# Optimization experiments

Hardware: AMD Instinct MI355X
Metric: run time of the kernel (lower is better)

The kernel has to match this reference:

```python
import jax, jax.numpy as jnp
import numpy as np

B, DIM, H, W = 8, 128, 64, 64
C, DI, N, R, K = DIM // 4, 2 * (DIM // 4), 16, 2, 4  # chunk dim, d_inner, d_state, dt_rank, n_dirs
L = H * W
EPS = 1e-5


def dwconv(x, w, b, dil):
    # x: [B,C,H,W]; w: [C,1,kh,kw] depthwise; torch padding='same' with dilation
    y = jax.lax.conv_general_dilated(
        x, w, window_strides=(1, 1), padding='SAME', rhs_dilation=(dil, dil),
        dimension_numbers=('NCHW', 'OIHW', 'NCHW'), feature_group_count=x.shape[1])
    return y + b[None, :, None, None]


def layernorm(x, w, b):
    mu = jnp.mean(x, -1, keepdims=True)
    var = jnp.var(x, -1, keepdims=True)
    return (x - mu) * jax.lax.rsqrt(var + EPS) * w + b


def axial_dw(x, mh_w, mh_b, mw_w, mw_b, c_w, c_b, dil):
    skip = x
    x = dwconv(x, mw_w, mw_b, dil)   # (1,7) kernel
    x = dwconv(x, mh_w, mh_b, dil)   # (7,1) kernel
    x = dwconv(x, c_w, c_b, dil)     # 3x3 kernel
    return x + skip


def ss2d(x, in_proj_w, conv_w, conv_b, x_proj_w, dt_proj_w, dt_proj_b,
         A_log, D, out_norm_w, out_norm_b, out_proj_w):
    # x: [B,H,W,C] channels-last (VMamba SS2D)
    b, h, w, _ = x.shape
    xz = jnp.einsum('bhwc,ec->bhwe', x, in_proj_w)          # [B,H,W,2*DI]
    xc, z = jnp.split(xz, 2, axis=-1)
    xc = xc.transpose(0, 3, 1, 2)                           # [B,DI,H,W]
    xc = jax.nn.silu(dwconv(xc, conv_w, conv_b, 1))
    l = h * w
    x_hw = xc.reshape(b, DI, l)
    x_wh = xc.transpose(0, 1, 3, 2).reshape(b, DI, l)
    xs = jnp.stack([x_hw, x_wh], 1)                         # [B,2,DI,L]
    xs = jnp.concatenate([xs, jnp.flip(xs, -1)], 1)         # [B,4,DI,L]
    x_dbl = jnp.einsum('bkdl,kcd->bkcl', xs, x_proj_w)      # c = R+2N
    dts, Bs, Cs = x_dbl[:, :, :R], x_dbl[:, :, R:R + N], x_dbl[:, :, R + N:]
    dts = jnp.einsum('bkrl,kdr->bkdl', dts, dt_proj_w)
    delta = jax.nn.softplus(dts + dt_proj_b[None, :, :, None])  # [B,4,DI,L]
    A = -jnp.exp(A_log)                                     # [4,DI,N]

    def step(hst, inp):
        u_t, dt_t, B_t, C_t = inp  # [B,4,DI],[B,4,DI],[B,4,N],[B,4,N]
        dA = jnp.exp(dt_t[..., None] * A)                   # [B,4,DI,N]
        hst = hst * dA + (dt_t * u_t)[..., None] * B_t[:, :, None, :]
        y = jnp.einsum('bkdn,bkn->bkd', hst, C_t)
        return hst, y

    u_l = jnp.moveaxis(xs, -1, 0)
    dt_l = jnp.moveaxis(delta, -1, 0)
    B_l = jnp.moveaxis(Bs, -1, 0)
    C_l = jnp.moveaxis(Cs, -1, 0)
    h0 = jnp.zeros((b, K, DI, N), xc.dtype)
    _, ys = jax.lax.scan(step, h0, (u_l, dt_l, B_l, C_l))   # [L,B,4,DI]
    out_y = jnp.moveaxis(ys, 0, -1) + D[None, :, :, None] * xs  # [B,4,DI,L]

    inv_y = jnp.flip(out_y[:, 2:4], -1)
    wh_y = out_y[:, 1].reshape(b, DI, w, h).transpose(0, 1, 3, 2).reshape(b, DI, l)
    invwh_y = inv_y[:, 1].reshape(b, DI, w, h).transpose(0, 1, 3, 2).reshape(b, DI, l)
    y = out_y[:, 0] + inv_y[:, 0] + wh_y + invwh_y          # [B,DI,L]
    y = y.transpose(0, 2, 1).reshape(b, h, w, DI)
    y = layernorm(y, out_norm_w, out_norm_b)
    y = y * jax.nn.silu(z)
    return jnp.einsum('bhwd,cd->bhwc', y, out_proj_w)


def setup_inputs() -> dict:
    key = jax.random.key(0)
    ks = iter(jax.random.split(key, 64))
    nrm = lambda s, sc=0.05: jax.random.normal(next(ks), s, jnp.float32) * sc
    inp = {'x': jax.random.normal(next(ks), (B, DIM, H, W), jnp.float32)}
    for i in (1, 2, 3):
        inp[f'dw{i}_mh_w'] = nrm((C, 1, 7, 1), 0.1); inp[f'dw{i}_mh_b'] = nrm((C,), 0.02)
        inp[f'dw{i}_mw_w'] = nrm((C, 1, 1, 7), 0.1); inp[f'dw{i}_mw_b'] = nrm((C,), 0.02)
        inp[f'dw{i}_c_w'] = nrm((C, 1, 3, 3), 0.1); inp[f'dw{i}_c_b'] = nrm((C,), 0.02)
    inp['ln_w'] = jnp.ones((C,)); inp['ln_b'] = jnp.zeros((C,))
    inp['in_proj_w'] = nrm((2 * DI, C))
    inp['conv_w'] = nrm((DI, 1, 3, 3), 0.1); inp['conv_b'] = nrm((DI,), 0.02)
    inp['x_proj_w'] = nrm((K, R + 2 * N, DI))
    inp['dt_proj_w'] = nrm((K, DI, R), 0.1)
    inp['dt_proj_b'] = nrm((K, DI), 0.02)
    inp['A_log'] = jax.random.uniform(next(ks), (K, DI, N), jnp.float32, 0.0, 2.0)
    inp['D'] = jnp.ones((K, DI), jnp.float32)
    inp['out_norm_w'] = jnp.ones((DI,)); inp['out_norm_b'] = jnp.zeros((DI,))
    inp['out_proj_w'] = nrm((C, DI))
    inp['bn_g'] = jnp.ones((DIM,)); inp['bn_b'] = jnp.zeros((DIM,))
    inp['bn_m'] = jnp.zeros((DIM,)); inp['bn_v'] = jnp.ones((DIM,))
    return inp


def reference(x, dw1_mh_w, dw1_mh_b, dw1_mw_w, dw1_mw_b, dw1_c_w, dw1_c_b,
              dw2_mh_w, dw2_mh_b, dw2_mw_w, dw2_mw_b, dw2_c_w, dw2_c_b,
              dw3_mh_w, dw3_mh_b, dw3_mw_w, dw3_mw_b, dw3_c_w, dw3_c_b,
              ln_w, ln_b, in_proj_w, conv_w, conv_b, x_proj_w, dt_proj_w, dt_proj_b,
              A_log, D, out_norm_w, out_norm_b, out_proj_w, bn_g, bn_b, bn_m, bn_v):
    def vss(xc):  # shared VSSBlock: [B,C,H,W] -> [B,C,H,W]
        t = xc.transpose(0, 2, 3, 1)
        t = t + ss2d(layernorm(t, ln_w, ln_b), in_proj_w, conv_w, conv_b, x_proj_w,
                     dt_proj_w, dt_proj_b, A_log, D, out_norm_w, out_norm_b, out_proj_w)
        return t.transpose(0, 3, 1, 2)

    x1, x2, x3, x4 = jnp.split(x, 4, axis=1)
    x1 = vss(axial_dw(x1, dw1_mh_w, dw1_mh_b, dw1_mw_w, dw1_mw_b, dw1_c_w, dw1_c_b, 1))
    x2 = vss(axial_dw(x2, dw2_mh_w, dw2_mh_b, dw2_mw_w, dw2_mw_b, dw2_c_w, dw2_c_b, 2))
    x3 = vss(axial_dw(x3, dw3_mh_w, dw3_mh_b, dw3_mw_w, dw3_mw_b, dw3_c_w, dw3_c_b, 3))
    xc = jnp.concatenate([x1, x2, x3, x4], axis=1)
    # BatchNorm2d in inference mode (running stats)
    y = (xc - bn_m[None, :, None, None]) * jax.lax.rsqrt(bn_v + EPS)[None, :, None, None]
    y = y * bn_g[None, :, None, None] + bn_b[None, :, None, None]
    return jax.nn.relu(y)
```

## Files before the change

### kernel.cpp

```cpp
#include <hip/hip_runtime.h>
#include <math.h>

#define LB __launch_bounds__(256)
#define LB512 __launch_bounds__(512)

#define LOG2E 1.44269504088896340736f
static __device__ __forceinline__ float silu_f(float x){ return x / (1.f + __expf(-x)); }
static __device__ __forceinline__ float softplus_f(float x){
    return (x > 20.f) ? x : __logf(1.f + __expf(x));
}

struct AxialArgs { const float* w[18]; };

__global__ LB void axial_kernel(const float* __restrict__ x, AxialArgs args,
                                float* __restrict__ acc)
{
    __shared__ float s0[4096];
    __shared__ float s1[4096];
    const int chunk = blockIdx.x >> 8;
    const int bc = blockIdx.x & 255;
    const int b = bc >> 5, c = bc & 31;
    const int dil = chunk + 1;
    const float* mh_w = args.w[chunk*6+0];
    const float* mh_b = args.w[chunk*6+1];
    const float* mw_w = args.w[chunk*6+2];
    const float* mw_b = args.w[chunk*6+3];
    const float* cw   = args.w[chunk*6+4];
    const float* cb   = args.w[chunk*6+5];
    const int tid = threadIdx.x;
    const float* xin = x + ((size_t)(b*128 + chunk*32 + c)) * 4096;
    float orig[16];
    #pragma unroll
    for (int kk=0;kk<16;++kk){ float v=xin[tid+kk*256]; orig[kk]=v; s0[tid+kk*256]=v; }
    __syncthreads();

    float w7[7];
    #pragma unroll
    for (int t=0;t<7;++t) w7[t]=mw_w[c*7+t];
    float bias = mw_b[c];
    float v[16];
    #pragma unroll
    for (int kk=0;kk<16;++kk){
        int p=tid+kk*256, i=p>>6, j=p&63;
        float s=bias;
        #pragma unroll
        for (int t=0;t<7;++t){ int jj=j+(t-3)*dil; if (jj>=0&&jj<64) s+=s0[i*64+jj]*w7[t]; }
        v[kk]=s;
    }
    #pragma unroll
    for (int kk=0;kk<16;++kk) s1[tid+kk*256]=v[kk];
    __syncthreads();

    #pragma unroll
    for (int t=0;t<7;++t) w7[t]=mh_w[c*7+t];
    bias = mh_b[c];
    #pragma unroll
    for (int kk=0;kk<16;++kk){
        int p=tid+kk*256, i=p>>6, j=p&63;
        float s=bias;
        #pragma unroll
        for (int t=0;t<7;++t){ int ii=i+(t-3)*dil; if (ii>=0&&ii<64) s+=s1[ii*64+j]*w7[t]; }
        v[kk]=s;
    }
    __syncthreads();
    #pragma unroll
    for (int kk=0;kk<16;++kk) s0[tid+kk*256]=v[kk];
    __syncthreads();

    float w9[9];
    #pragma unroll
    for (int t=0;t<9;++t) w9[t]=cw[c*9+t];
    bias = cb[c];
    float* aout = acc + (size_t)chunk*1048576 + ((size_t)(b*32+c))*4096;
    #pragma unroll
    for (int kk=0;kk<16;++kk){
        int p=tid+kk*256, i=p>>6, j=p&63;
        float s=bias;
        #pragma unroll
        for (int a=0;a<3;++a){
            int ii=i+(a-1)*dil; if (ii<0||ii>=64) continue;
            #pragma unroll
            for (int bb2=0;bb2<3;++bb2){
                int jj=j+(bb2-1)*dil; if (jj<0||jj>=64) continue;
                s += s0[ii*64+jj]*w9[a*3+bb2];
            }
        }
        aout[p] = s + orig[kk];
    }
}

__global__ LB512 void lnproj_kernel(const float* __restrict__ acc,
    const float* __restrict__ ln_w, const float* __restrict__ ln_b,
    const float* __restrict__ in_proj_w,
    float* __restrict__ xc, float* __restrict__ z)
{
    __shared__ float s_a[32*65];
    const int b = blockIdx.x >> 6, lt = blockIdx.x & 63;
    const int l0 = lt*64;
    const int tid = threadIdx.x;
    const float* ab = acc + (size_t)b*32*4096 + l0;
    for (int i=tid;i<2048;i+=512){ int c=i>>6, j=i&63; s_a[c*65+j]=ab[(size_t)c*4096 + j]; }
    __syncthreads();
    const int l = tid & 63;
    const int g = __builtin_amdgcn_readfirstlane(tid >> 6);
    float v[32];
    float mu=0.f;
    #pragma unroll
    for (int c=0;c<32;++c){ v[c]=s_a[c*65+l]; mu+=v[c]; }
    mu *= (1.f/32.f);
    float var=0.f;
    #pragma unroll
    for (int c=0;c<32;++c){ float d2=v[c]-mu; var+=d2*d2; }
    var *= (1.f/32.f);
    float rs = rsqrtf(var+1e-5f);
    #pragma unroll
    for (int c=0;c<32;++c) v[c] = (v[c]-mu)*rs*ln_w[c] + ln_b[c];
    float* xcp = xc + (size_t)b*64*4096 + l0 + l;
    float* zp  = z  + (size_t)b*64*4096 + l0 + l;
    for (int e=g*16; e<g*16+16; ++e){
        const float* wr = in_proj_w + e*32;
        float s=0.f;
        #pragma unroll
        for (int c=0;c<32;++c) s += wr[c]*v[c];
        if (e<64) xcp[(size_t)e*4096]=s; else zp[(size_t)(e-64)*4096]=s;
    }
}

__global__ LB void conv3_kernel(const float* __restrict__ xc,
    const float* __restrict__ conv_w, const float* __restrict__ conv_b,
    float* __restrict__ xconv, float* __restrict__ xconvT)
{
    __shared__ float s0[4096];
    __shared__ float s1[64*65];
    const int bd = blockIdx.x;
    const int d = bd & 63;
    const int tid = threadIdx.x;
    const float* in = xc + (size_t)bd*4096;
    #pragma unroll
    for (int kk=0;kk<16;++kk) s0[tid+kk*256]=in[tid+kk*256];
    __syncthreads();
    float w9[9];
    #pragma unroll
    for (int t=0;t<9;++t) w9[t]=conv_w[d*9+t];
    float bias = conv_b[d];
    float* outp = xconv + (size_t)bd*4096;
    #pragma unroll
    for (int kk=0;kk<16;++kk){
        int p=tid+kk*256, i=p>>6, j=p&63;
        float s=bias;
        #pragma unroll
        for (int a=0;a<3;++a){
            int ii=i+a-1; if (ii<0||ii>=64) continue;
            #pragma unroll
            for (int bb2=0;bb2<3;++bb2){
                int jj=j+bb2-1; if (jj<0||jj>=64) continue;
                s += s0[ii*64+jj]*w9[a*3+bb2];
            }
        }
        s = silu_f(s);
        outp[p]=s;
        s1[i*65+j]=s;
    }
    __syncthreads();
    float* outT = xconvT + (size_t)bd*4096;
    #pragma unroll
    for (int kk=0;kk<16;++kk){ int p=tid+kk*256; outT[p] = s1[(p&63)*65 + (p>>6)]; }
}

__global__ LB void projscan1_kernel(const float* __restrict__ xconv, const float* __restrict__ xconvT,
    const float* __restrict__ x_proj_w, const float* __restrict__ dt_proj_w,
    const float* __restrict__ dt_proj_b, const float* __restrict__ A_log,
    float* __restrict__ Bsb, float* __restrict__ Csb, float* __restrict__ dts_g,
    float* __restrict__ Ssum, float* __restrict__ hloc)
{
    __shared__ float s_x[64*65];
    __shared__ float s_dlt[64*65];
    __shared__ __align__(16) float s_B[1024];
    __shared__ float s_dts[128];
    __shared__ float s_Spart[4][64];
    float* s_C = s_dlt;
    const int blk = blockIdx.x;
    const int g = blk & 63, bk = blk >> 6;
    const int k = bk & 3, b = bk >> 2;
    const int tid = threadIdx.x;
    const int t0 = g*64;
    const float* src = (k & 1) ? xconvT : xconv;
    const float* sb = src + (size_t)b*64*4096;
    for (int i=tid;i<4096;i+=256){
        int d=i>>6, j=i&63;
        int col = (k&2) ? (4095-(t0+j)) : (t0+j);
        s_x[j*65+d] = sb[(size_t)d*4096 + col];
    }
    __syncthreads();

    {
        const int t = tid & 63;
        const int q = __builtin_amdgcn_readfirstlane(tid >> 6);
        const float* wp = x_proj_w + k*2176;
        float acc9[9];
        #pragma unroll
        for (int r=0;r<9;++r) acc9[r]=0.f;
        const int r0 = q*9;
        const int nr = (q==3)?7:9;
        for (int ch=0; ch<4; ++ch){
            float xv[16];
            #pragma unroll
            for (int i=0;i<16;++i) xv[i] = s_x[t*65 + ch*16 + i];
            #pragma unroll
            for (int r=0;r<9;++r){
                if (r < nr){
                    const float* wr = wp + (r0+r)*64 + ch*16;
                    float s=0.f;
                    #pragma unroll
                    for (int i=0;i<16;++i) s += wr[i]*xv[i];
                    acc9[r] += s;
                }
            }
        }
        #pragma unroll
        for (int r=0;r<9;++r){
            if (r<nr){
                int row = r0 + r;
                if (row < 2)       s_dts[t*2 + row]      = acc9[r];
                else if (row < 18) s_B[t*16 + (row-2)]   = acc9[r];
                else               s_C[t*16 + (row-18)]  = acc9[r];
            }
        }
    }
    __syncthreads();

    {
        const size_t tb = (size_t)blk*1024;
        for (int i=tid;i<1024;i+=256){ Bsb[tb+i]=s_B[i]; Csb[tb+i]=s_C[i]; }
        if (tid<128) dts_g[(size_t)blk*128 + tid] = s_dts[tid];
    }
    __syncthreads();

    {
        const int d_ = tid & 63, part = tid >> 6;
        const float w0 = dt_proj_w[k*128 + d_*2], w1 = dt_proj_w[k*128 + d_*2 + 1];
        const float bb = dt_proj_b[k*64 + d_];
        float Sp = 0.f;
        #pragma unroll
        for (int i=0;i<16;++i){
            const int t = part*16 + i;
            float dlt = softplus_f(s_dts[t*2]*w0 + s_dts[t*2+1]*w1 + bb);
            s_dlt[t*65 + d_] = dlt;
            s_x[t*65 + d_] *= dlt;
            Sp += dlt;
        }
        s_Spart[part][d_] = Sp;
    }
    __syncthreads();
    if (tid < 64){
        Ssum[(size_t)blk*64 + tid] = s_Spart[0][tid]+s_Spart[1][tid]
                                   + s_Spart[2][tid]+s_Spart[3][tid];
    }

    const int d = tid >> 2, nb = (tid & 3)*4;
    float4 Av = *(const float4*)(A_log + ((size_t)(k*64+d)*16 + nb));
    const float A0 = -__expf(Av.x)*LOG2E, A1 = -__expf(Av.y)*LOG2E,
                A2 = -__expf(Av.z)*LOG2E, A3 = -__expf(Av.w)*LOG2E;
    float h0=0,h1=0,h2=0,h3=0;
    #pragma unroll 4
    for (int t=0;t<64;++t){
        float dlt = s_dlt[t*65+d];
        float du  = s_x[t*65+d];
        float4 Bv = *(const float4*)&s_B[t*16+nb];
        h0 = h0*exp2f(dlt*A0) + du*Bv.x;
        h1 = h1*exp2f(dlt*A1) + du*Bv.y;
        h2 = h2*exp2f(dlt*A2) + du*Bv.z;
        h3 = h3*exp2f(dlt*A3) + du*Bv.w;
    }
    ((float4*)hloc)[(size_t)blk*256 + tid] = make_float4(h0,h1,h2,h3);
}

__global__ LB void scan2_kernel(const float* __restrict__ Ssum,
    const float* __restrict__ hloc, const float* __restrict__ A_log,
    float* __restrict__ hin)
{
    const int j = blockIdx.x*256 + threadIdx.x;
    const int bk = j >> 10, dn = j & 1023;
    const int k = bk & 3, d = dn >> 4, n = dn & 15;
    const float A = -__expf(A_log[(size_t)(k*64+d)*16 + n]) * LOG2E;
    float h = 0.f;
    for (int g=0; g<64; ++g){
        const size_t o = ((size_t)bk*64 + g)*1024 + dn;
        hin[o] = h;
        float S = Ssum[((size_t)bk*64 + g)*64 + d];
        h = exp2f(A*S)*h + hloc[o];
    }
}

__global__ LB void scan3_kernel(const float* __restrict__ xconv, const float* __restrict__ xconvT,
    const float* __restrict__ Bsb, const float* __restrict__ Csb,
    const float* __restrict__ dts_g,
    const float* __restrict__ dt_proj_w, const float* __restrict__ dt_proj_b,
    const float* __restrict__ A_log, const float* __restrict__ Dp,
    const float* __restrict__ hin, float* __restrict__ outy)
{
    __shared__ __align__(16) float s_B[4][1024];
    __shared__ __align__(16) float s_C[4][1024];
    __shared__ float s_dts[4][128];
    __shared__ float s_y[4][64*17];
    const int w = threadIdx.x >> 6;
    const int lane = threadIdx.x & 63;
    const int tile = blockIdx.x*4 + w;
    const int g = tile & 63, bk = tile >> 6;
    const int k = bk & 3, b = bk >> 2;

    {
        const float4* B4 = (const float4*)(Bsb + (size_t)tile*1024);
        const float4* C4 = (const float4*)(Csb + (size_t)tile*1024);
        float4* sB4 = (float4*)s_B[w];
        float4* sC4 = (float4*)s_C[w];
        #pragma unroll
        for (int qq=0;qq<4;++qq){ sB4[lane+64*qq]=B4[lane+64*qq]; sC4[lane+64*qq]=C4[lane+64*qq]; }
        s_dts[w][lane]      = dts_g[(size_t)tile*128 + lane];
        s_dts[w][lane+64]   = dts_g[(size_t)tile*128 + lane + 64];
    }
    const int d = lane;
    float A[16];
    {
        const float* Ab = A_log + (size_t)(k*64+d)*16;
        #pragma unroll
        for (int n=0;n<16;++n) A[n] = -__expf(Ab[n])*LOG2E;
    }
    float h[16];
    {
        const float4* hb = (const float4*)(hin + (size_t)tile*1024 + d*16);
        #pragma unroll
        for (int qq=0;qq<4;++qq){
            float4 v=hb[qq];
            h[qq*4+0]=v.x; h[qq*4+1]=v.y; h[qq*4+2]=v.z; h[qq*4+3]=v.w;
        }
    }
    const float w0 = dt_proj_w[k*128 + d*2], w1 = dt_proj_w[k*128 + d*2 + 1];
    const float bb = dt_proj_b[k*64 + d];
    const float Dv = Dp[k*64 + d];
    const float* up = ((k&1)?xconvT:xconv) + (size_t)(b*64+d)*4096;
    const float4* sB4 = (const float4*)s_B[w];
    const float4* sC4 = (const float4*)s_C[w];
    float* syw = s_y[w];

    for (int t4=0; t4<16; ++t4){
        float u4[4];
        if (k & 2){
            float4 r = *(const float4*)(up + (4092 - g*64 - t4*4));
            u4[0]=r.w; u4[1]=r.z; u4[2]=r.y; u4[3]=r.x;
        } else {
            float4 r = *(const float4*)(up + g*64 + t4*4);
            u4[0]=r.x; u4[1]=r.y; u4[2]=r.z; u4[3]=r.w;
        }
        #pragma unroll
        for (int j=0;j<4;++j){
            const int t = t4*4 + j;
            float dt0 = s_dts[w][t*2], dt1 = s_dts[w][t*2+1];
            float dlt = softplus_f(dt0*w0 + dt1*w1 + bb);
            float du  = dlt * u4[j];
            float y = 0.f;
            #pragma unroll
            for (int qq=0;qq<4;++qq){
                float4 Bv = sB4[t*4+qq];
                float4 Cv = sC4[t*4+qq];
                h[qq*4+0] = h[qq*4+0]*exp2f(dlt*A[qq*4+0]) + du*Bv.x;
                h[qq*4+1] = h[qq*4+1]*exp2f(dlt*A[qq*4+1]) + du*Bv.y;
                h[qq*4+2] = h[qq*4+2]*exp2f(dlt*A[qq*4+2]) + du*Bv.z;
                h[qq*4+3] = h[qq*4+3]*exp2f(dlt*A[qq*4+3]) + du*Bv.w;
                y += h[qq*4+0]*Cv.x + h[qq*4+1]*Cv.y + h[qq*4+2]*Cv.z + h[qq*4+3]*Cv.w;
            }
            syw[d*17 + (t & 15)] = y + Dv*u4[j];
        }
        if ((t4 & 3) == 3){
            const int tb = t4 >> 2;
            #pragma unroll
            for (int qq=0;qq<16;++qq){
                int i = qq*64 + lane;
                int dd = i >> 4, jj = i & 15;
                outy[((size_t)(bk*64+dd))*4096 + g*64 + tb*16 + jj] = syw[dd*17 + jj];
            }
        }
    }
}

__global__ LB void outyT_kernel(const float* __restrict__ outy, float* __restrict__ outyT)
{
    __shared__ float s[64*65];
    const int p = blockIdx.x;
    const int kk = p >> 9, bd = p & 511;
    const int b = bd >> 6, d = bd & 63;
    const float* ip = outy + ((size_t)(b*4 + (kk?3:1))*64 + d)*4096;
    const int tid = threadIdx.x;
    #pragma unroll
    for (int k2=0;k2<16;++k2){ int pp=tid+k2*256; s[(pp>>6)*65+(pp&63)] = ip[pp]; }
    __syncthreads();
    float* op = outyT + ((size_t)(kk*8+b)*64 + d)*4096;
    #pragma unroll
    for (int k2=0;k2<16;++k2){ int pp=tid+k2*256; op[pp] = s[(pp&63)*65 + (pp>>6)]; }
}

__global__ LB512 void combine_kernel(const float* __restrict__ outy,
    const float* __restrict__ outyT,
    const float* __restrict__ z, const float* __restrict__ acc,
    const float* __restrict__ onw, const float* __restrict__ onb,
    const float* __restrict__ opw,
    const float* __restrict__ bn_g, const float* __restrict__ bn_b,
    const float* __restrict__ bn_m, const float* __restrict__ bn_v,
    int c_off, float* __restrict__ out)
{
    __shared__ float s_red[2][8][64];
    __shared__ float s_y[64*65];
    const int b = blockIdx.x >> 6, lt = blockIdx.x & 63;
    const int l0 = lt*64;
    const int tid = threadIdx.x;
    const int l = tid & 63;
    const int g = __builtin_amdgcn_readfirstlane(tid >> 6);
    const float* o0 = outy  + (size_t)(b*4+0)*64*4096;
    const float* o2 = outy  + (size_t)(b*4+2)*64*4096;
    const float* T1 = outyT + (size_t)(0*8+b)*64*4096;
    const float* T3 = outyT + (size_t)(1*8+b)*64*4096;
    const int lf = l0 + l;
    const int lr = 4095 - lf;
    float y[8];
    float psum=0.f, psq=0.f;
    #pragma unroll
    for (int i=0;i<8;++i){
        int d = g*8+i;
        float vv = o0[(size_t)d*4096 + lf] + o2[(size_t)d*4096 + lr]
                 + T1[(size_t)d*4096 + lf] + T3[(size_t)d*4096 + lr];
        y[i]=vv; psum+=vv; psq+=vv*vv;
    }
    s_red[0][g][l]=psum; s_red[1][g][l]=psq;
    __syncthreads();
    float mu=0.f, vsum=0.f;
    #pragma unroll
    for (int gg=0;gg<8;++gg){ mu += s_red[0][gg][l]; vsum += s_red[1][gg][l]; }
    mu *= (1.f/64.f);
    float var = vsum*(1.f/64.f) - mu*mu;
    float rs = rsqrtf(var + 1e-5f);
    const float* zp = z + (size_t)b*64*4096 + lf;
    #pragma unroll
    for (int i=0;i<8;++i){
        int d = g*8+i;
        float t2 = (y[i]-mu)*rs*onw[d] + onb[d];
        float zv = zp[(size_t)d*4096];
        s_y[l*65 + d] = t2 * silu_f(zv);
    }
    __syncthreads();
    float a4[4] = {0.f,0.f,0.f,0.f};
    for (int d=0; d<64; ++d){
        float xval = s_y[l*65+d];
        #pragma unroll
        for (int j=0;j<4;++j) a4[j] += opw[(g*4+j)*64+d]*xval;
    }
    const float* ap = acc + (size_t)b*32*4096 + lf;
    #pragma unroll
    for (int j=0;j<4;++j){
        int c = g*4+j, ch = c_off+c;
        float s = a4[j] + ap[(size_t)c*4096];
        float bnv = (s - bn_m[ch])*rsqrtf(bn_v[ch]+1e-5f)*bn_g[ch] + bn_b[ch];
        out[((size_t)b*128+ch)*4096 + lf] = fmaxf(bnv, 0.f);
    }
}

__global__ LB void bnpass_kernel(const float* __restrict__ x,
    const float* __restrict__ bn_g, const float* __restrict__ bn_b,
    const float* __restrict__ bn_m, const float* __restrict__ bn_v,
    float* __restrict__ out)
{
    const int gid = blockIdx.x*256 + threadIdx.x;
    const int l = gid & 4095, bc = gid >> 12;
    const int c = bc & 31, b = bc >> 5;
    const int ch = 96 + c;
    const size_t idx = ((size_t)b*128+ch)*4096 + l;
    float v = x[idx];
    float r = (v - bn_m[ch])*rsqrtf(bn_v[ch]+1e-5f)*bn_g[ch] + bn_b[ch];
    out[idx] = fmaxf(r, 0.f);
}

extern "C" void kernel_launch(void* const* d_in, const int* in_sizes, int n_in,
                              void* d_out, int out_size, void* d_ws, size_t ws_size,
                              hipStream_t stream) {
    const float* x         = (const float*)d_in[0];
    const float* ln_w      = (const float*)d_in[19];
    const float* ln_b      = (const float*)d_in[20];
    const float* in_proj_w = (const float*)d_in[21];
    const float* conv_w    = (const float*)d_in[22];
    const float* conv_b    = (const float*)d_in[23];
    const float* x_proj_w  = (const float*)d_in[24];
    const float* dt_proj_w = (const float*)d_in[25];
    const float* dt_proj_b = (const float*)d_in[26];
    const float* A_log     = (const float*)d_in[27];
    const float* Dp        = (const float*)d_in[28];
    const float* onw       = (const float*)d_in[29];
    const float* onb       = (const float*)d_in[30];
    const float* opw       = (const float*)d_in[31];
    const float* bn_g      = (const float*)d_in[32];
    const float* bn_b      = (const float*)d_in[33];
    const float* bn_m      = (const float*)d_in[34];
    const float* bn_v      = (const float*)d_in[35];
    float* out = (float*)d_out;

    float* ws = (float*)d_ws;
    float* acc    = ws;
    float* xc     = acc    + 3145728;
    float* z      = xc     + 2097152;
    float* xconv  = z      + 2097152;
    float* xconvT = xconv  + 2097152;
    float* Bsb    = xconvT + 2097152;
    float* Csb    = Bsb    + 2097152;
    float* dts_g  = Csb    + 2097152;
    float* Ssum   = dts_g  + 262144;
    float* hlo    = Ssum   + 131072;
    float* hin    = hlo    + 2097152;
    float* outy   = hin    + 2097152;
    float* outyT  = outy   + 8388608;

    bnpass_kernel<<<4096, 256, 0, stream>>>(x, bn_g, bn_b, bn_m, bn_v, out);

    AxialArgs aargs;
    for (int chunk=0; chunk<3; ++chunk)
        for (int jj=0; jj<6; ++jj)
            aargs.w[chunk*6+jj] = (const float*)d_in[1 + chunk*6 + jj];
    axial_kernel<<<768, 256, 0, stream>>>(x, aargs, acc);

    for (int chunk=0; chunk<3; ++chunk){
        const int c_off = chunk*32;
        const float* acc_c = acc + (size_t)chunk*1048576;

        lnproj_kernel<<<512, 512, 0, stream>>>(acc_c, ln_w, ln_b, in_proj_w, xc, z);
        conv3_kernel<<<512, 256, 0, stream>>>(xc, conv_w, conv_b, xconv, xconvT);
        projscan1_kernel<<<2048, 256, 0, stream>>>(xconv, xconvT, x_proj_w, dt_proj_w, dt_proj_b,
                                                   A_log, Bsb, Csb, dts_g, Ssum, hlo);
        scan2_kernel<<<128, 256, 0, stream>>>(Ssum, hlo, A_log, hin);
        scan3_kernel<<<512, 256, 0, stream>>>(xconv, xconvT, Bsb, Csb, dts_g,
                                              dt_proj_w, dt_proj_b, A_log, Dp, hin, outy);
        outyT_kernel<<<1024, 256, 0, stream>>>(outy, outyT);
        combine_kernel<<<512, 512, 0, stream>>>(outy, outyT, z, acc_c, onw, onb, opw,
                                                bn_g, bn_b, bn_m, bn_v, c_off, out);
    }
}
```

Baseline: 512.9 us.

## Batch the three chunks into single launches and restructure scan and reduction kernels

Kernels for the three VSS chunks are now launched once with three times the grid, with per-chunk workspace strides, whenever the workspace is large enough; otherwise the per-chunk loop remains. projscan1 drops its shared delta buffer and computes softplus inline, reading u straight from global memory with a per-wave state split. scan3 writes outputs as float4 directly instead of staging through shared memory, and a new reduce4 kernel sums the four directions, replacing the outyT transpose so combine reads a single buffer. The aim is more parallelism per launch and fewer launches and memory passes, at the cost of a much larger workspace and a fallback path that depends on its size.

```diff
diff --git a/kernel.cpp b/kernel.cpp
--- a/kernel.cpp
+++ b/kernel.cpp
@@ -89,16 +89,19 @@
     }
 }
 
-__global__ LB512 void lnproj_kernel(const float* __restrict__ acc,
+__global__ LB512 void lnproj_kernel(const float* __restrict__ acc, int ch0, size_t cs,
     const float* __restrict__ ln_w, const float* __restrict__ ln_b,
     const float* __restrict__ in_proj_w,
     float* __restrict__ xc, float* __restrict__ z)
 {
     __shared__ float s_a[32*65];
-    const int b = blockIdx.x >> 6, lt = blockIdx.x & 63;
+    const int cl = blockIdx.x >> 9;
+    const int local = blockIdx.x & 511;
+    const int chunk = ch0 + cl;
+    const int b = local >> 6, lt = local & 63;
     const int l0 = lt*64;
     const int tid = threadIdx.x;
-    const float* ab = acc + (size_t)b*32*4096 + l0;
+    const float* ab = acc + (size_t)chunk*1048576 + (size_t)b*32*4096 + l0;
     for (int i=tid;i<2048;i+=512){ int c=i>>6, j=i&63; s_a[c*65+j]=ab[(size_t)c*4096 + j]; }
     __syncthreads();
     const int l = tid & 63;
@@ -115,8 +118,8 @@
     float rs = rsqrtf(var+1e-5f);
     #pragma unroll
     for (int c=0;c<32;++c) v[c] = (v[c]-mu)*rs*ln_w[c] + ln_b[c];
-    float* xcp = xc + (size_t)b*64*4096 + l0 + l;
-    float* zp  = z  + (size_t)b*64*4096 + l0 + l;
+    float* xcp = xc + (size_t)cl*cs + (size_t)b*64*4096 + l0 + l;
+    float* zp  = z  + (size_t)cl*cs + (size_t)b*64*4096 + l0 + l;
     for (int e=g*16; e<g*16+16; ++e){
         const float* wr = in_proj_w + e*32;
         float s=0.f;
@@ -126,16 +129,17 @@
     }
 }
 
-__global__ LB void conv3_kernel(const float* __restrict__ xc,
+__global__ LB void conv3_kernel(const float* __restrict__ xc, size_t cs,
     const float* __restrict__ conv_w, const float* __restrict__ conv_b,
     float* __restrict__ xconv, float* __restrict__ xconvT)
 {
     __shared__ float s0[4096];
     __shared__ float s1[64*65];
-    const int bd = blockIdx.x;
+    const int cl = blockIdx.x >> 9;
+    const int bd = blockIdx.x & 511;
     const int d = bd & 63;
     const int tid = threadIdx.x;
-    const float* in = xc + (size_t)bd*4096;
+    const float* in = xc + (size_t)cl*cs + (size_t)bd*4096;
     #pragma unroll
     for (int kk=0;kk<16;++kk) s0[tid+kk*256]=in[tid+kk*256];
     __syncthreads();
@@ -143,7 +147,7 @@
     #pragma unroll
     for (int t=0;t<9;++t) w9[t]=conv_w[d*9+t];
     float bias = conv_b[d];
-    float* outp = xconv + (size_t)bd*4096;
+    float* outp = xconv + (size_t)cl*cs + (size_t)bd*4096;
     #pragma unroll
     for (int kk=0;kk<16;++kk){
         int p=tid+kk*256, i=p>>6, j=p&63;
@@ -162,29 +166,29 @@
         s1[i*65+j]=s;
     }
     __syncthreads();
-    float* outT = xconvT + (size_t)bd*4096;
+    float* outT = xconvT + (size_t)cl*cs + (size_t)bd*4096;
     #pragma unroll
     for (int kk=0;kk<16;++kk){ int p=tid+kk*256; outT[p] = s1[(p&63)*65 + (p>>6)]; }
 }
 
 __global__ LB void projscan1_kernel(const float* __restrict__ xconv, const float* __restrict__ xconvT,
+    size_t cs,
     const float* __restrict__ x_proj_w, const float* __restrict__ dt_proj_w,
     const float* __restrict__ dt_proj_b, const float* __restrict__ A_log,
     float* __restrict__ Bsb, float* __restrict__ Csb, float* __restrict__ dts_g,
     float* __restrict__ Ssum, float* __restrict__ hloc)
 {
     __shared__ float s_x[64*65];
-    __shared__ float s_dlt[64*65];
     __shared__ __align__(16) float s_B[1024];
+    __shared__ __align__(16) float s_C[1024];
     __shared__ float s_dts[128];
-    __shared__ float s_Spart[4][64];
-    float* s_C = s_dlt;
-    const int blk = blockIdx.x;
-    const int g = blk & 63, bk = blk >> 6;
+    const int cl = blockIdx.x >> 11;
+    const int blkL = blockIdx.x & 2047;
+    const int g = blkL & 63, bk = blkL >> 6;
     const int k = bk & 3, b = bk >> 2;
     const int tid = threadIdx.x;
     const int t0 = g*64;
-    const float* src = (k & 1) ? xconvT : xconv;
+    const float* src = ((k & 1) ? xconvT : xconv) + (size_t)cl*cs;
     const float* sb = src + (size_t)b*64*4096;
     for (int i=tid;i<4096;i+=256){
         int d=i>>6, j=i&63;
@@ -230,119 +234,23 @@
     __syncthreads();
 
     {
-        const size_t tb = (size_t)blk*1024;
-        for (int i=tid;i<1024;i+=256){ Bsb[tb+i]=s_B[i]; Csb[tb+i]=s_C[i]; }
-        if (tid<128) dts_g[(size_t)blk*128 + tid] = s_dts[tid];
-    }
-    __syncthreads();
-
-    {
-        const int d_ = tid & 63, part = tid >> 6;
-        const float w0 = dt_proj_w[k*128 + d_*2], w1 = dt_proj_w[k*128 + d_*2 + 1];
-        const float bb = dt_proj_b[k*64 + d_];
-        float Sp = 0.f;
-        #pragma unroll
-        for (int i=0;i<16;++i){
-            const int t = part*16 + i;
-            float dlt = softplus_f(s_dts[t*2]*w0 + s_dts[t*2+1]*w1 + bb);
-            s_dlt[t*65 + d_] = dlt;
-            s_x[t*65 + d_] *= dlt;
-            Sp += dlt;
-        }
-        s_Spart[part][d_] = Sp;
-    }
-    __syncthreads();
-    if (tid < 64){
-        Ssum[(size_t)blk*64 + tid] = s_Spart[0][tid]+s_Spart[1][tid]
-                                   + s_Spart[2][tid]+s_Spart[3][tid];
-    }
-
-    const int d = tid >> 2, nb = (tid & 3)*4;
-    float4 Av = *(const float4*)(A_log + ((size_t)(k*64+d)*16 + nb));
+        float* BsbC = Bsb + (size_t)cl*cs;
+        float* CsbC = Csb + (size_t)cl*cs;
+        const size_t tb = (size_t)blkL*1024;
+        for (int i=tid;i<1024;i+=256){ BsbC[tb+i]=s_B[i]; CsbC[tb+i]=s_C[i]; }
+        if (tid<128) (dts_g + (size_t)cl*cs)[(size_t)blkL*128 + tid] = s_dts[tid];
+    }
+
+    const int d = tid & 63;
+    const int w = tid >> 6;
+    float4 Av = *(const float4*)(A_log + ((size_t)(k*64+d)*16 + w*4));
     const float A0 = -__expf(Av.x)*LOG2E, A1 = -__expf(Av.y)*LOG2E,
                 A2 = -__expf(Av.z)*LOG2E, A3 = -__expf(Av.w)*LOG2E;
-    float h0=0,h1=0,h2=0,h3=0;
-    #pragma unroll 4
-    for (int t=0;t<64;++t){
-        float dlt = s_dlt[t*65+d];
-        float du  = s_x[t*65+d];
-        float4 Bv = *(const float4*)&s_B[t*16+nb];
-        h0 = h0*exp2f(dlt*A0) + du*Bv.x;
-        h1 = h1*exp2f(dlt*A1) + du*Bv.y;
-        h2 = h2*exp2f(dlt*A2) + du*Bv.z;
-        h3 = h3*exp2f(dlt*A3) + du*Bv.w;
-    }
-    ((float4*)hloc)[(size_t)blk*256 + tid] = make_float4(h0,h1,h2,h3);
-}
-
-__global__ LB void scan2_kernel(const float* __restrict__ Ssum,
-    const float* __restrict__ hloc, const float* __restrict__ A_log,
-    float* __restrict__ hin)
-{
-    const int j = blockIdx.x*256 + threadIdx.x;
-    const int bk = j >> 10, dn = j & 1023;
-    const int k = bk & 3, d = dn >> 4, n = dn & 15;
-    const float A = -__expf(A_log[(size_t)(k*64+d)*16 + n]) * LOG2E;
-    float h = 0.f;
-    for (int g=0; g<64; ++g){
-        const size_t o = ((size_t)bk*64 + g)*1024 + dn;
-        hin[o] = h;
-        float S = Ssum[((size_t)bk*64 + g)*64 + d];
-        h = exp2f(A*S)*h + hloc[o];
-    }
-}
-
-__global__ LB void scan3_kernel(const float* __restrict__ xconv, const float* __restrict__ xconvT,
-    const float* __restrict__ Bsb, const float* __restrict__ Csb,
-    const float* __restrict__ dts_g,
-    const float* __restrict__ dt_proj_w, const float* __restrict__ dt_proj_b,
-    const float* __restrict__ A_log, const float* __restrict__ Dp,
-    const float* __restrict__ hin, float* __restrict__ outy)
-{
-    __shared__ __align__(16) float s_B[4][1024];
-    __shared__ __align__(16) float s_C[4][1024];
-    __shared__ float s_dts[4][128];
-    __shared__ float s_y[4][64*17];
-    const int w = threadIdx.x >> 6;
-    const int lane = threadIdx.x & 63;
-    const int tile = blockIdx.x*4 + w;
-    const int g = tile & 63, bk = tile >> 6;
-    const int k = bk & 3, b = bk >> 2;
-
-    {
-        const float4* B4 = (const float4*)(Bsb + (size_t)tile*1024);
-        const float4* C4 = (const float4*)(Csb + (size_t)tile*1024);
-        float4* sB4 = (float4*)s_B[w];
-        float4* sC4 = (float4*)s_C[w];
-        #pragma unroll
-        for (int qq=0;qq<4;++qq){ sB4[lane+64*qq]=B4[lane+64*qq]; sC4[lane+64*qq]=C4[lane+64*qq]; }
-        s_dts[w][lane]      = dts_g[(size_t)tile*128 + lane];
-        s_dts[w][lane+64]   = dts_g[(size_t)tile*128 + lane + 64];
-    }
-    const int d = lane;
-    float A[16];
-    {
-        const float* Ab = A_log + (size_t)(k*64+d)*16;
-        #pragma unroll
-        for (int n=0;n<16;++n) A[n] = -__expf(Ab[n])*LOG2E;
-    }
-    float h[16];
-    {
-        const float4* hb = (const float4*)(hin + (size_t)tile*1024 + d*16);
-        #pragma unroll
-        for (int qq=0;qq<4;++qq){
-            float4 v=hb[qq];
-            h[qq*4+0]=v.x; h[qq*4+1]=v.y; h[qq*4+2]=v.z; h[qq*4+3]=v.w;
-        }
-    }
     const float w0 = dt_proj_w[k*128 + d*2], w1 = dt_proj_w[k*128 + d*2 + 1];
     const float bb = dt_proj_b[k*64 + d];
-    const float Dv = Dp[k*64 + d];
-    const float* up = ((k&1)?xconvT:xconv) + (size_t)(b*64+d)*4096;
-    const float4* sB4 = (const float4*)s_B[w];
-    const float4* sC4 = (const float4*)s_C[w];
-    float* syw = s_y[w];
-
+    const float* up = src + (size_t)(b*64+d)*4096;
+    const float4* sB4 = (const float4*)s_B;
+    float h0=0,h1=0,h2=0,h3=0, S=0.f;
     for (int t4=0; t4<16; ++t4){
         float u4[4];
         if (k & 2){
@@ -352,6 +260,107 @@
             float4 r = *(const float4*)(up + g*64 + t4*4);
             u4[0]=r.x; u4[1]=r.y; u4[2]=r.z; u4[3]=r.w;
         }
+        #pragma unroll
+        for (int j=0;j<4;++j){
+            const int t = t4*4 + j;
+            float dlt = softplus_f(s_dts[t*2]*w0 + s_dts[t*2+1]*w1 + bb);
+            S += dlt;
+            float du = dlt * u4[j];
+            float4 Bv = sB4[t*4 + w];
+            h0 = h0*exp2f(dlt*A0) + du*Bv.x;
+            h1 = h1*exp2f(dlt*A1) + du*Bv.y;
+            h2 = h2*exp2f(dlt*A2) + du*Bv.z;
+            h3 = h3*exp2f(dlt*A3) + du*Bv.w;
+        }
+    }
+    if (w == 0) (Ssum + (size_t)cl*cs)[(size_t)blkL*64 + d] = S;
+    ((float4*)(hloc + (size_t)cl*cs))[(size_t)blkL*256 + d*4 + w] = make_float4(h0,h1,h2,h3);
+}
+
+__global__ LB void scan2_kernel(const float* __restrict__ Ssum, size_t cs,
+    const float* __restrict__ hloc, const float* __restrict__ A_log,
+    float* __restrict__ hin)
+{
+    const int cl = blockIdx.x >> 7;
+    const int j = (blockIdx.x & 127)*256 + threadIdx.x;
+    const int bk = j >> 10, dn = j & 1023;
+    const int k = bk & 3, d = dn >> 4, n = dn & 15;
+    const float* SsC = Ssum + (size_t)cl*cs;
+    const float* hlC = hloc + (size_t)cl*cs;
+    float* hinC = hin + (size_t)cl*cs;
+    const float A = -__expf(A_log[(size_t)(k*64+d)*16 + n]) * LOG2E;
+    float h = 0.f;
+    for (int g=0; g<64; ++g){
+        const size_t o = ((size_t)bk*64 + g)*1024 + dn;
+        hinC[o] = h;
+        float S = SsC[((size_t)bk*64 + g)*64 + d];
+        h = exp2f(A*S)*h + hlC[o];
+    }
+}
+
+__global__ LB void scan3_kernel(const float* __restrict__ xconv, const float* __restrict__ xconvT,
+    size_t cs,
+    const float* __restrict__ Bsb, const float* __restrict__ Csb,
+    const float* __restrict__ dts_g,
+    const float* __restrict__ dt_proj_w, const float* __restrict__ dt_proj_b,
+    const float* __restrict__ A_log, const float* __restrict__ Dp,
+    const float* __restrict__ hin, float* __restrict__ outy)
+{
+    __shared__ __align__(16) float s_B[4][1024];
+    __shared__ __align__(16) float s_C[4][1024];
+    __shared__ float s_dts[4][128];
+    const int cl = blockIdx.x >> 9;
+    const int w = threadIdx.x >> 6;
+    const int lane = threadIdx.x & 63;
+    const int tile = (blockIdx.x & 511)*4 + w;
+    const int g = tile & 63, bk = tile >> 6;
+    const int k = bk & 3, b = bk >> 2;
+
+    {
+        const float4* B4 = (const float4*)(Bsb + (size_t)cl*cs + (size_t)tile*1024);
+        const float4* C4 = (const float4*)(Csb + (size_t)cl*cs + (size_t)tile*1024);
+        float4* sB4 = (float4*)s_B[w];
+        float4* sC4 = (float4*)s_C[w];
+        #pragma unroll
+        for (int qq=0;qq<4;++qq){ sB4[lane+64*qq]=B4[lane+64*qq]; sC4[lane+64*qq]=C4[lane+64*qq]; }
+        const float* dtsC = dts_g + (size_t)cl*cs;
+        s_dts[w][lane]      = dtsC[(size_t)tile*128 + lane];
+        s_dts[w][lane+64]   = dtsC[(size_t)tile*128 + lane + 64];
+    }
+    const int d = lane;
+    float A[16];
+    {
+        const float* Ab = A_log + (size_t)(k*64+d)*16;
+        #pragma unroll
+        for (int n=0;n<16;++n) A[n] = -__expf(Ab[n])*LOG2E;
+    }
+    float h[16];
+    {
+        const float4* hb = (const float4*)(hin + (size_t)cl*cs + (size_t)tile*1024 + d*16);
+        #pragma unroll
+        for (int qq=0;qq<4;++qq){
+            float4 v=hb[qq];
+            h[qq*4+0]=v.x; h[qq*4+1]=v.y; h[qq*4+2]=v.z; h[qq*4+3]=v.w;
+        }
+    }
+    const float w0 = dt_proj_w[k*128 + d*2], w1 = dt_proj_w[k*128 + d*2 + 1];
+    const float bb = dt_proj_b[k*64 + d];
+    const float Dv = Dp[k*64 + d];
+    const float* up = ((k&1)?xconvT:xconv) + (size_t)cl*cs + (size_t)(b*64+d)*4096;
+    const float4* sB4 = (const float4*)s_B[w];
+    const float4* sC4 = (const float4*)s_C[w];
+    float* orow = outy + (size_t)cl*cs + ((size_t)(bk*64 + d))*4096 + g*64;
+
+    for (int t4=0; t4<16; ++t4){
+        float u4[4];
+        if (k & 2){
+            float4 r = *(const float4*)(up + (4092 - g*64 - t4*4));
+            u4[0]=r.w; u4[1]=r.z; u4[2]=r.y; u4[3]=r.x;
+        } else {
+            float4 r = *(const float4*)(up + g*64 + t4*4);
+            u4[0]=r.x; u4[1]=r.y; u4[2]=r.z; u4[3]=r.w;
+        }
+        float y4[4];
         #pragma unroll
         for (int j=0;j<4;++j){
             const int t = t4*4 + j;
@@ -369,65 +378,68 @@
                 h[qq*4+3] = h[qq*4+3]*exp2f(dlt*A[qq*4+3]) + du*Bv.w;
                 y += h[qq*4+0]*Cv.x + h[qq*4+1]*Cv.y + h[qq*4+2]*Cv.z + h[qq*4+3]*Cv.w;
             }
-            syw[d*17 + (t & 15)] = y + Dv*u4[j];
-        }
-        if ((t4 & 3) == 3){
-            const int tb = t4 >> 2;
-            #pragma unroll
-            for (int qq=0;qq<16;++qq){
-                int i = qq*64 + lane;
-                int dd = i >> 4, jj = i & 15;
-                outy[((size_t)(bk*64+dd))*4096 + g*64 + tb*16 + jj] = syw[dd*17 + jj];
-            }
-        }
-    }
-}
-
-__global__ LB void outyT_kernel(const float* __restrict__ outy, float* __restrict__ outyT)
-{
-    __shared__ float s[64*65];
-    const int p = blockIdx.x;
-    const int kk = p >> 9, bd = p & 511;
-    const int b = bd >> 6, d = bd & 63;
-    const float* ip = outy + ((size_t)(b*4 + (kk?3:1))*64 + d)*4096;
+            y4[j] = y + Dv*u4[j];
+        }
+        *(float4*)(orow + t4*4) = make_float4(y4[0],y4[1],y4[2],y4[3]);
+    }
+}
+
+__global__ LB void reduce4_kernel(const float* __restrict__ outy, size_t cs,
+                                  float* __restrict__ ysum)
+{
+    __shared__ float s1[64*65];
+    __shared__ float s3[64*65];
+    const int cl = blockIdx.x >> 9;
+    const int local = blockIdx.x & 511;
+    const int b = local >> 6, d = local & 63;
     const int tid = threadIdx.x;
-    #pragma unroll
-    for (int k2=0;k2<16;++k2){ int pp=tid+k2*256; s[(pp>>6)*65+(pp&63)] = ip[pp]; }
-    __syncthreads();
-    float* op = outyT + ((size_t)(kk*8+b)*64 + d)*4096;
-    #pragma unroll
-    for (int k2=0;k2<16;++k2){ int pp=tid+k2*256; op[pp] = s[(pp&63)*65 + (pp>>6)]; }
-}
-
-__global__ LB512 void combine_kernel(const float* __restrict__ outy,
-    const float* __restrict__ outyT,
+    const float* oy = outy + (size_t)cl*cs;
+    const float* o0 = oy + ((size_t)((b*4+0)*64 + d))*4096;
+    const float* o1 = oy + ((size_t)((b*4+1)*64 + d))*4096;
+    const float* o2 = oy + ((size_t)((b*4+2)*64 + d))*4096;
+    const float* o3 = oy + ((size_t)((b*4+3)*64 + d))*4096;
+    #pragma unroll
+    for (int it=0; it<16; ++it){
+        int p = tid + it*256;
+        s1[(p>>6)*65 + (p&63)] = o1[p];
+        s3[(p>>6)*65 + (p&63)] = o3[p];
+    }
+    __syncthreads();
+    float* ys = ysum + (size_t)cl*cs + ((size_t)(b*64 + d))*4096;
+    #pragma unroll
+    for (int it=0; it<16; ++it){
+        int p = tid + it*256;
+        int i = p >> 6, j = p & 63;
+        ys[p] = o0[p] + o2[4095-p] + s1[j*65 + i] + s3[(63-j)*65 + (63-i)];
+    }
+}
+
+__global__ LB512 void combine_kernel(const float* __restrict__ ysum, int ch0, size_t cs,
     const float* __restrict__ z, const float* __restrict__ acc,
     const float* __restrict__ onw, const float* __restrict__ onb,
     const float* __restrict__ opw,
     const float* __restrict__ bn_g, const float* __restrict__ bn_b,
     const float* __restrict__ bn_m, const float* __restrict__ bn_v,
-    int c_off, float* __restrict__ out)
+    float* __restrict__ out)
 {
     __shared__ float s_red[2][8][64];
     __shared__ float s_y[64*65];
-    const int b = blockIdx.x >> 6, lt = blockIdx.x & 63;
+    const int cl = blockIdx.x >> 9;
+    const int chunk = ch0 + cl;
+    const int local = blockIdx.x & 511;
+    const int b = local >> 6, lt = local & 63;
     const int l0 = lt*64;
     const int tid = threadIdx.x;
     const int l = tid & 63;
     const int g = __builtin_amdgcn_readfirstlane(tid >> 6);
-    const float* o0 = outy  + (size_t)(b*4+0)*64*4096;
-    const float* o2 = outy  + (size_t)(b*4+2)*64*4096;
-    const float* T1 = outyT + (size_t)(0*8+b)*64*4096;
-    const float* T3 = outyT + (size_t)(1*8+b)*64*4096;
+    const float* ys = ysum + (size_t)cl*cs + (size_t)b*64*4096;
     const int lf = l0 + l;
-    const int lr = 4095 - lf;
     float y[8];
     float psum=0.f, psq=0.f;
     #pragma unroll
     for (int i=0;i<8;++i){
         int d = g*8+i;
-        float vv = o0[(size_t)d*4096 + lf] + o2[(size_t)d*4096 + lr]
-                 + T1[(size_t)d*4096 + lf] + T3[(size_t)d*4096 + lr];
+        float vv = ys[(size_t)d*4096 + lf];
         y[i]=vv; psum+=vv; psq+=vv*vv;
     }
     s_red[0][g][l]=psum; s_red[1][g][l]=psq;
@@ -438,7 +450,7 @@
     mu *= (1.f/64.f);
     float var = vsum*(1.f/64.f) - mu*mu;
     float rs = rsqrtf(var + 1e-5f);
-    const float* zp = z + (size_t)b*64*4096 + lf;
+    const float* zp = z + (size_t)cl*cs + (size_t)b*64*4096 + lf;
     #pragma unroll
     for (int i=0;i<8;++i){
         int d = g*8+i;
@@ -453,10 +465,10 @@
         #pragma unroll
         for (int j=0;j<4;++j) a4[j] += opw[(g*4+j)*64+d]*xval;
     }
-    const float* ap = acc + (size_t)b*32*4096 + lf;
+    const float* ap = acc + (size_t)chunk*1048576 + (size_t)b*32*4096 + lf;
     #pragma unroll
     for (int j=0;j<4;++j){
-        int c = g*4+j, ch = c_off+c;
+        int c = g*4+j, ch = chunk*32 + c;
         float s = a4[j] + ap[(size_t)c*4096];
         float bnv = (s - bn_m[ch])*rsqrtf(bn_v[ch]+1e-5f)*bn_g[ch] + bn_b[ch];
         out[((size_t)b*128+ch)*4096 + lf] = fmaxf(bnv, 0.f);
@@ -501,20 +513,40 @@
     const float* bn_v      = (const float*)d_in[35];
     float* out = (float*)d_out;
 
+    const size_t F_XC   = 0;
+    const size_t F_Z    = 2097152;
+    const size_t F_XCV  = 4194304;
+    const size_t F_XCVT = 6291456;
+    const size_t F_BSB  = 8388608;
+    const size_t F_CSB  = 10485760;
+    const size_t F_DTS  = 12582912;
+    const size_t F_SSUM = 12845056;
+    const size_t F_HLO  = 12976128;
+    const size_t F_HIN  = 15073280;
+    const size_t F_OUTY = 17170432;
+    const size_t F_YSUM = 25559040;
+    const size_t CSF    = 27656192;
+
     float* ws = (float*)d_ws;
-    float* acc    = ws;
-    float* xc     = acc    + 3145728;
-    float* z      = xc     + 2097152;
-    float* xconv  = z      + 2097152;
-    float* xconvT = xconv  + 2097152;
-    float* Bsb    = xconvT + 2097152;
-    float* Csb    = Bsb    + 2097152;
-    float* dts_g  = Csb    + 2097152;
-    float* Ssum   = dts_g  + 262144;
-    float* hlo    = Ssum   + 131072;
-    float* hin    = hlo    + 2097152;
-    float* outy   = hin    + 2097152;
-    float* outyT  = outy   + 8388608;
+    float* acc  = ws;
+    float* pool = acc + 3145728;
+
+    const bool batch = ws_size >= (size_t)(3145728 + 3*CSF) * sizeof(float);
+    const int  nch   = batch ? 3 : 1;
+    const size_t cs  = batch ? CSF : 0;
+
+    float* xc     = pool + F_XC;
+    float* z      = pool + F_Z;
+    float* xconv  = pool + F_XCV;
+    float* xconvT = pool + F_XCVT;
+    float* Bsb    = pool + F_BSB;
+    float* Csb    = pool + F_CSB;
+    float* dts_g  = pool + F_DTS;
+    float* Ssum   = pool + F_SSUM;
+    float* hlo    = pool + F_HLO;
+    float* hin    = pool + F_HIN;
+    float* outy   = pool + F_OUTY;
+    float* ysum   = pool + F_YSUM;
 
     bnpass_kernel<<<4096, 256, 0, stream>>>(x, bn_g, bn_b, bn_m, bn_v, out);
 
@@ -524,19 +556,20 @@
             aargs.w[chunk*6+jj] = (const float*)d_in[1 + chunk*6 + jj];
     axial_kernel<<<768, 256, 0, stream>>>(x, aargs, acc);
 
-    for (int chunk=0; chunk<3; ++chunk){
-        const int c_off = chunk*32;
-        const float* acc_c = acc + (size_t)chunk*1048576;
-
-        lnproj_kernel<<<512, 512, 0, stream>>>(acc_c, ln_w, ln_b, in_proj_w, xc, z);
-        conv3_kernel<<<512, 256, 0, stream>>>(xc, conv_w, conv_b, xconv, xconvT);
-        projscan1_kernel<<<2048, 256, 0, stream>>>(xconv, xconvT, x_proj_w, dt_proj_w, dt_proj_b,
-                                                   A_log, Bsb, Csb, dts_g, Ssum, hlo);
-        scan2_kernel<<<128, 256, 0, stream>>>(Ssum, hlo, A_log, hin);
-        scan3_kernel<<<512, 256, 0, stream>>>(xconv, xconvT, Bsb, Csb, dts_g,
-                                              dt_proj_w, dt_proj_b, A_log, Dp, hin, outy);
-        outyT_kernel<<<1024, 256, 0, stream>>>(outy, outyT);
-        combine_kernel<<<512, 512, 0, stream>>>(outy, outyT, z, acc_c, onw, onb, opw,
-                                                bn_g, bn_b, bn_m, bn_v, c_off, out);
-    }
-}
+    const int nloop = batch ? 1 : 3;
+    for (int it=0; it<nloop; ++it){
+        const int ch0 = batch ? 0 : it;
+
+        lnproj_kernel<<<nch*512, 512, 0, stream>>>(acc, ch0, cs, ln_w, ln_b, in_proj_w, xc, z);
+        conv3_kernel<<<nch*512, 256, 0, stream>>>(xc, cs, conv_w, conv_b, xconv, xconvT);
+        projscan1_kernel<<<nch*2048, 256, 0, stream>>>(xconv, xconvT, cs,
+                                                       x_proj_w, dt_proj_w, dt_proj_b,
+                                                       A_log, Bsb, Csb, dts_g, Ssum, hlo);
+        scan2_kernel<<<nch*128, 256, 0, stream>>>(Ssum, cs, hlo, A_log, hin);
+        scan3_kernel<<<nch*512, 256, 0, stream>>>(xconv, xconvT, cs, Bsb, Csb, dts_g,
+                                                  dt_proj_w, dt_proj_b, A_log, Dp, hin, outy);
+        reduce4_kernel<<<nch*512, 256, 0, stream>>>(outy, cs, ysum);
+        combine_kernel<<<nch*512, 512, 0, stream>>>(ysum, ch0, cs, z, acc, onw, onb, opw,
+                                                    bn_g, bn_b, bn_m, bn_v, out);
+    }
+}
```

After: 576.3 us. 12.3% more time.
